# Performance work log

Hardware: AMD Instinct MI355X
Metric: run time of the kernel (lower is better)

Reference implementation:

```python
import jax, jax.numpy as jnp
from jax import lax
import numpy as np

EPS_BN = 1e-5


def _bn(x, g, b, axis):
    # eval-mode BatchNorm with running_mean=0, running_var=1
    shape = [1] * x.ndim
    shape[axis] = -1
    scale = (g / jnp.sqrt(1.0 + EPS_BN)).reshape(shape)
    return x * scale + b.reshape(shape)


def farthest_point_sample(xyz, npoint):
    B, N, _ = xyz.shape
    bidx = jnp.arange(B)

    def body(carry, _):
        dist, far = carry                      # [B,N], [B]
        centroid = xyz[bidx, far]              # [B,3]
        d = jnp.sum((xyz - centroid[:, None, :]) ** 2, axis=-1)
        dist = jnp.minimum(dist, d)
        return (dist, jnp.argmax(dist, axis=-1)), far

    init = (jnp.full((B, N), 1e10, xyz.dtype), jnp.zeros((B,), jnp.int32))
    _, idxs = lax.scan(body, init, None, length=npoint)
    return idxs.T                              # [B,npoint]


def square_distance(src, dst):
    # [B,S,3] x [B,N,3] -> [B,S,N]
    d = -2.0 * jnp.einsum('bsc,bnc->bsn', src, dst)
    d = d + jnp.sum(src ** 2, -1)[:, :, None] + jnp.sum(dst ** 2, -1)[:, None, :]
    return d


def sample_and_group(npoint, nsample, xyz, points):
    B = xyz.shape[0]
    bidx = jnp.arange(B)
    fps_idx = farthest_point_sample(xyz, npoint)          # [B,S]
    new_xyz = xyz[bidx[:, None], fps_idx]                 # [B,S,3]
    new_points = points[bidx[:, None], fps_idx]           # [B,S,C]
    dists = square_distance(new_xyz, xyz)                 # [B,S,N]
    _, idx = lax.top_k(-dists, nsample)                   # nearest nsample
    grouped = points[bidx[:, None, None], idx]            # [B,S,K,C]
    grouped_norm = grouped - new_points[:, :, None, :]
    rep = jnp.broadcast_to(new_points[:, :, None, :], grouped.shape)
    return new_xyz, jnp.concatenate([grouped_norm, rep], axis=-1)  # [B,S,K,2C]


def local_op(x, w, g, b):
    # x [B,S,K,D]; conv1d k=1 over channels D, BN, ReLU, max over K -> [B,out,S]
    y = jnp.einsum('bskd,od->bsko', x, w)
    y = jax.nn.relu(_bn(y, g, b, axis=3))
    y = jnp.max(y, axis=2)                                # [B,S,out]
    return jnp.transpose(y, (0, 2, 1))                    # [B,out,S]


def sa_layer(x, qk_w, v_w, v_b, t_w, t_b, g, b):
    # x [B,C,N]; q and k share weights (offset attention)
    xq = jnp.einsum('bcn,oc->bno', x, qk_w)               # [B,N,C/4]
    xk = jnp.einsum('bcn,oc->bon', x, qk_w)               # [B,C/4,N]
    xv = jnp.einsum('bcn,oc->bon', x, v_w) + v_b[:, None]
    energy = jnp.einsum('bnd,bdm->bnm', xq, xk)           # [B,N,N]
    attn = jax.nn.softmax(energy, axis=-1)
    attn = attn / (1e-9 + attn.sum(axis=1, keepdims=True))
    x_r = jnp.einsum('bcn,bnm->bcm', xv, attn)
    x_r = jnp.einsum('bcn,oc->bon', x - x_r, t_w) + t_b[:, None]
    x_r = jax.nn.relu(_bn(x_r, g, b, axis=1))
    return x + x_r


def setup_inputs() -> dict:
    key = jax.random.key(0)
    ks = iter(jax.random.split(key, 48))
    rn = lambda shape, s=0.05: jax.random.normal(next(ks), shape, jnp.float32) * s
    inp = {
        'xyz': jax.random.normal(next(ks), (32, 16384, 3), jnp.float32),
        'f': jax.random.normal(next(ks), (32, 16384, 3), jnp.float32),
        'conv1_w': rn((64, 6)), 'bn1_g': jnp.ones(64), 'bn1_b': jnp.zeros(64),
        'l0_w': rn((64, 128)), 'l0_g': jnp.ones(64), 'l0_b': jnp.zeros(64),
        'l1_w': rn((64, 128)), 'l1_g': jnp.ones(64), 'l1_b': jnp.zeros(64),
        'st_c1_w': rn((64, 64)), 'st_bn1_g': jnp.ones(64), 'st_bn1_b': jnp.zeros(64),
        'st_c2_w': rn((64, 64)), 'st_bn2_g': jnp.ones(64), 'st_bn2_b': jnp.zeros(64),
        'sa1_qk_w': rn((16, 64)), 'sa1_v_w': rn((64, 64)), 'sa1_v_b': jnp.zeros(64),
        'sa1_t_w': rn((64, 64)), 'sa1_t_b': jnp.zeros(64), 'sa1_g': jnp.ones(64), 'sa1_b': jnp.zeros(64),
        'sa2_qk_w': rn((16, 64)), 'sa2_v_w': rn((64, 64)), 'sa2_v_b': jnp.zeros(64),
        'sa2_t_w': rn((64, 64)), 'sa2_t_b': jnp.zeros(64), 'sa2_g': jnp.ones(64), 'sa2_b': jnp.zeros(64),
        'fuse_w': rn((256, 192)), 'fuse_g': jnp.ones(256), 'fuse_b': jnp.zeros(256),
        'lin1_w': rn((256, 256)), 'bn6_g': jnp.ones(256), 'bn6_b': jnp.zeros(256),
        'lin2_w': rn((256, 256)), 'lin2_b': jnp.zeros(256),
    }
    return inp


def _forward(xyz, f, conv1_w, bn1_g, bn1_b, l0_w, l0_g, l0_b, l1_w, l1_g, l1_b,
             st_c1_w, st_bn1_g, st_bn1_b, st_c2_w, st_bn2_g, st_bn2_b,
             sa1_qk_w, sa1_v_w, sa1_v_b, sa1_t_w, sa1_t_b, sa1_g, sa1_b,
             sa2_qk_w, sa2_v_w, sa2_v_b, sa2_t_w, sa2_t_b, sa2_g, sa2_b,
             fuse_w, fuse_g, fuse_b, lin1_w, bn6_g, bn6_b, lin2_w, lin2_b):
    center = jnp.mean(xyz, axis=1)                        # [B,3]
    xyz_c = xyz - center[:, None, :]
    pts = jnp.concatenate([xyz_c, f], axis=2)             # [B,N,6]
    geo = pts[..., :3]
    xin = jnp.transpose(pts, (0, 2, 1))                   # [B,6,N]
    x = jax.nn.relu(_bn(jnp.einsum('bcn,oc->bon', xin, conv1_w), bn1_g, bn1_b, 1))
    x = jnp.transpose(x, (0, 2, 1))                       # [B,N,64]
    new_xyz, nf = sample_and_group(128, 32, geo, x)
    feature_0 = local_op(nf, l0_w, l0_g, l0_b)            # [B,64,128]
    feature = jnp.transpose(feature_0, (0, 2, 1))
    _, nf2 = sample_and_group(32, 16, new_xyz, feature)
    feature_1 = local_op(nf2, l1_w, l1_g, l1_b)           # [B,64,32]
    # StackedAttention
    x = jax.nn.relu(_bn(jnp.einsum('bcn,oc->bon', feature_1, st_c1_w), st_bn1_g, st_bn1_b, 1))
    x = jax.nn.relu(_bn(jnp.einsum('bcn,oc->bon', x, st_c2_w), st_bn2_g, st_bn2_b, 1))
    x1 = sa_layer(x, sa1_qk_w, sa1_v_w, sa1_v_b, sa1_t_w, sa1_t_b, sa1_g, sa1_b)
    x2 = sa_layer(x1, sa2_qk_w, sa2_v_w, sa2_v_b, sa2_t_w, sa2_t_b, sa2_g, sa2_b)
    x = jnp.concatenate([x1, x2], axis=1)                 # [B,128,32]
    x = jnp.concatenate([x, feature_1], axis=1)           # [B,192,32]
    x = jax.nn.leaky_relu(_bn(jnp.einsum('bcn,oc->bon', x, fuse_w), fuse_g, fuse_b, 1), 0.2)
    x = jnp.max(x, axis=2)                                # [B,256]
    x = jax.nn.relu(_bn(x @ lin1_w.T, bn6_g, bn6_b, 1))   # dropout = identity (eval)
    x = x @ lin2_w.T + lin2_b
    return center, x


def reference(xyz, f, conv1_w, bn1_g, bn1_b, l0_w, l0_g, l0_b, l1_w, l1_g, l1_b,
              st_c1_w, st_bn1_g, st_bn1_b, st_c2_w, st_bn2_g, st_bn2_b,
              sa1_qk_w, sa1_v_w, sa1_v_b, sa1_t_w, sa1_t_b, sa1_g, sa1_b,
              sa2_qk_w, sa2_v_w, sa2_v_b, sa2_t_w, sa2_t_b, sa2_g, sa2_b,
              fuse_w, fuse_g, fuse_b, lin1_w, bn6_g, bn6_b, lin2_w, lin2_b):
    return _forward(xyz, f, conv1_w, bn1_g, bn1_b, l0_w, l0_g, l0_b, l1_w, l1_g, l1_b,
                    st_c1_w, st_bn1_g, st_bn1_b, st_c2_w, st_bn2_g, st_bn2_b,
                    sa1_qk_w, sa1_v_w, sa1_v_b, sa1_t_w, sa1_t_b, sa1_g, sa1_b,
                    sa2_qk_w, sa2_v_w, sa2_v_b, sa2_t_w, sa2_t_b, sa2_g, sa2_b,
                    fuse_w, fuse_g, fuse_b, lin1_w, bn6_g, bn6_b, lin2_w, lin2_b)
```

## Files before the change

kernel.cpp:

```cpp
#include <hip/hip_runtime.h>


__device__ __forceinline__ float bnscale(float g){ return g / sqrtf(1.0f + 1e-5f); }

__device__ __forceinline__ float conv_feat6(float p0,float p1,float p2,float p3,float p4,float p5,
                                            float w0,float w1,float w2,float w3,float w4,float w5,
                                            float sc,float bs){
    float y = p0*w0;
    y = fmaf(p1,w1,y); y = fmaf(p2,w2,y); y = fmaf(p3,w3,y);
    y = fmaf(p4,w4,y); y = fmaf(p5,w5,y);
    return fmaxf(fmaf(y,sc,bs), 0.0f);
}

__device__ __forceinline__ float fpsdist(float dx,float dy,float dz){
    #pragma clang fp contract(off)
    return (dx*dx + dy*dy) + dz*dz;
}

__device__ __forceinline__ float sumsq3(float x,float y,float z){
    #pragma clang fp contract(off)
    return (x*x + y*y) + z*z;
}
__device__ __forceinline__ float sqdist3(float qx,float qy,float qz,float qs,
                                         float px,float py,float pz){
    #pragma clang fp contract(off)
    {
        float dot = (qx*px + qy*py) + qz*pz;
        float pn  = (px*px + py*py) + pz*pz;
        return (-2.0f*dot + qs) + pn;
    }
}

__device__ __forceinline__ unsigned long long packdi(float d, unsigned int idx){
    unsigned int u = __float_as_uint(d);
    unsigned int msk = (unsigned int)((int)u >> 31);
    u ^= (msk | 0x80000000u);
    return ((unsigned long long)u << 32) | (unsigned long long)idx;
}

__device__ __forceinline__ unsigned long long u64min(unsigned long long a, unsigned long long b){
    return a < b ? a : b;
}

__device__ __forceinline__ unsigned long long u64_shfl_down(unsigned long long v, int off){
    unsigned int lo = (unsigned int)v, hi = (unsigned int)(v >> 32);
    lo = __shfl_down(lo, off, 64);
    hi = __shfl_down(hi, off, 64);
    return ((unsigned long long)hi << 32) | (unsigned long long)lo;
}

__device__ __forceinline__ unsigned long long u64_bcast0(unsigned long long v){
    unsigned int lo = (unsigned int)v, hi = (unsigned int)(v >> 32);
    lo = __shfl(lo, 0, 64);
    hi = __shfl(hi, 0, 64);
    return ((unsigned long long)hi << 32) | (unsigned long long)lo;
}

__global__ __launch_bounds__(256) void k_center(const float* __restrict__ xyz,
                                                float* __restrict__ center,
                                                float* __restrict__ out){
    int b = blockIdx.x, t = threadIdx.x;
    __shared__ float sb[256][3];
    float sx=0.f, sy=0.f, sz=0.f;
    for (int n = t; n < 16384; n += 256){
        const float* p = xyz + ((size_t)b*16384 + n)*3;
        sx += p[0]; sy += p[1]; sz += p[2];
    }
    sb[t][0]=sx; sb[t][1]=sy; sb[t][2]=sz;
    __syncthreads();
    for (int off=128; off; off>>=1){
        if (t < off){ sb[t][0]+=sb[t+off][0]; sb[t][1]+=sb[t+off][1]; sb[t][2]+=sb[t+off][2]; }
        __syncthreads();
    }
    if (t < 3){
        float c = sb[0][t] / 16384.0f;
        center[b*3+t] = c;
        out[b*3+t] = c;
    }
}

template<int N, int NPOINT, int NTH, int PPT, bool SUB>
__global__ __launch_bounds__(NTH) void k_fps(const float* __restrict__ src,
                                             const float* __restrict__ center,
                                             int* __restrict__ idx_out){
    static_assert(N == NTH*PPT, "bad fps cfg");
    constexpr int NW = NTH/64;
    int b = blockIdx.x, t = threadIdx.x;
    int wid = t>>6, lane = t&63;

    __shared__ unsigned int s_khi[2][NW], s_klo[2][NW];
    __shared__ float s_wx[2][NW], s_wy[2][NW], s_wz[2][NW];
    __shared__ float s_c0[3];

    float cx0=0.f, cy0=0.f, cz0=0.f;
    if constexpr (SUB){
        cx0 = center[b*3+0]; cy0 = center[b*3+1]; cz0 = center[b*3+2];
    }
    float px[PPT], py[PPT], pz[PPT], dist[PPT];
    #pragma unroll
    for (int i=0;i<PPT;i++){
        int p = t + i*NTH;
        const float* sp = src + ((size_t)b*N + p)*3;
        px[i]=sp[0]-cx0; py[i]=sp[1]-cy0; pz[i]=sp[2]-cz0;
        dist[i]=1e10f;
    }
    if (t==0){
        idx_out[b*NPOINT] = 0;
        s_c0[0]=px[0]; s_c0[1]=py[0]; s_c0[2]=pz[0];
    }
    __syncthreads();
    float cx=s_c0[0], cy=s_c0[1], cz=s_c0[2];

    for (int it=1; it<NPOINT; ++it){
        int par = it & 1;
        float bv = -1.0f; int bi = 0;
        float bx = 0.f, by = 0.f, bz = 0.f;
        #pragma unroll
        for (int i=0;i<PPT;i++){
            float d = fpsdist(px[i]-cx, py[i]-cy, pz[i]-cz);
            float nd = fminf(dist[i], d);
            dist[i] = nd;
            bool better = nd > bv;
            bv = better ? nd : bv;
            bi = better ? (t + i*NTH) : bi;
            bx = better ? px[i] : bx;
            by = better ? py[i] : by;
            bz = better ? pz[i] : bz;
        }
        unsigned long long key = ((unsigned long long)__float_as_uint(bv) << 32)
                               | (unsigned long long)(unsigned)(~(unsigned)bi);
        #pragma unroll
        for (int off=32; off>=1; off>>=1){
            unsigned long long ok = u64_shfl_down(key, off);
            float ox = __shfl_down(bx, off, 64);
            float oy = __shfl_down(by, off, 64);
            float oz = __shfl_down(bz, off, 64);
            bool better = ok > key;
            key = better ? ok : key;
            bx  = better ? ox : bx;
            by  = better ? oy : by;
            bz  = better ? oz : bz;
        }
        if (lane==0){
            s_khi[par][wid] = (unsigned)(key >> 32);
            s_klo[par][wid] = (unsigned)key;
            s_wx[par][wid]  = bx;
            s_wy[par][wid]  = by;
            s_wz[par][wid]  = bz;
        }
        __syncthreads();
        unsigned long long gk = ((unsigned long long)s_khi[par][0] << 32) | s_klo[par][0];
        int gw = 0;
        #pragma unroll
        for (int w2=1; w2<NW; ++w2){
            unsigned long long k2 = ((unsigned long long)s_khi[par][w2] << 32) | s_klo[par][w2];
            if (k2 > gk){ gk = k2; gw = w2; }
        }
        cx = s_wx[par][gw]; cy = s_wy[par][gw]; cz = s_wz[par][gw];
        if (t==0) idx_out[b*NPOINT + it] = (int)(~(unsigned)(gk & 0xFFFFFFFFull));
    }
}

__global__ __launch_bounds__(64) void k_gather1(const float* __restrict__ xyz,
                                                const float* __restrict__ f,
                                                const float* __restrict__ center,
                                                const float* __restrict__ conv1_w,
                                                const float* __restrict__ bn1_g,
                                                const float* __restrict__ bn1_b,
                                                const int* __restrict__ fps_idx,
                                                float* __restrict__ new_xyz,
                                                float* __restrict__ np_feat){
    int q = blockIdx.x; int b = q>>7, s = q&127;
    int o = threadIdx.x;
    int idx = fps_idx[b*128+s];
    const float* xp = xyz + ((size_t)b*16384 + idx)*3;
    const float* fp = f   + ((size_t)b*16384 + idx)*3;
    float p0 = xp[0]-center[b*3+0], p1 = xp[1]-center[b*3+1], p2 = xp[2]-center[b*3+2];
    float p3 = fp[0], p4 = fp[1], p5 = fp[2];
    const float* w = conv1_w + o*6;
    float v = conv_feat6(p0,p1,p2,p3,p4,p5, w[0],w[1],w[2],w[3],w[4],w[5],
                         bnscale(bn1_g[o]), bn1_b[o]);
    np_feat[((size_t)b*128 + s)*64 + o] = v;
    if (o < 3){
        float pc = (o==0)?p0:((o==1)?p1:p2);
        new_xyz[((size_t)b*128 + s)*3 + o] = pc;
    }
}

__global__ __launch_bounds__(256) void k_knn1(const float* __restrict__ xyz,
                                              const float* __restrict__ center,
                                              const float* __restrict__ new_xyz,
                                              int* __restrict__ knn_idx){
    int q = blockIdx.x; int b = q>>7;
    int t = threadIdx.x;
    __shared__ unsigned long long scmin[256];

    float cx = center[b*3+0], cy = center[b*3+1], cz = center[b*3+2];
    float qx = new_xyz[(size_t)q*3+0], qy = new_xyz[(size_t)q*3+1], qz = new_xyz[(size_t)q*3+2];
    float qs = sumsq3(qx,qy,qz);
    const float* xb = xyz + (size_t)b*16384*3;

    unsigned long long m = 0xFFFFFFFFFFFFFFFFull;
    for (int i=0;i<64;i++){
        int n = t + (i<<8);
        const float* p = xb + (size_t)n*3;
        float px = p[0]-cx, py = p[1]-cy, pz = p[2]-cz;
        float d = sqdist3(qx,qy,qz,qs,px,py,pz);
        m = u64min(m, packdi(d, (unsigned)n));
    }
    scmin[t] = m;
    __syncthreads();
    if (t >= 64) return;

    for (int r=0; r<32; ++r){
        unsigned long long mm = u64min(u64min(scmin[t], scmin[t+64]),
                                       u64min(scmin[t+128], scmin[t+192]));
        #pragma unroll
        for (int off=32; off>=1; off>>=1) mm = u64min(mm, u64_shfl_down(mm, off));
        unsigned long long win = u64_bcast0(mm);
        unsigned int widx = (unsigned int)(win & 0xFFFFFFFFull);
        if (t==0) knn_idx[(size_t)q*32 + r] = (int)widx;
        int c = (int)(widx & 255u);
        int n = c + (t<<8);
        const float* p = xb + (size_t)n*3;
        float px = p[0]-cx, py = p[1]-cy, pz = p[2]-cz;
        float d = sqdist3(qx,qy,qz,qs,px,py,pz);
        unsigned long long pk = packdi(d, (unsigned)n);
        if (pk <= win) pk = 0xFFFFFFFFFFFFFFFFull;
        #pragma unroll
        for (int off=32; off>=1; off>>=1) pk = u64min(pk, u64_shfl_down(pk, off));
        if (t==0) scmin[c] = pk;
    }
}

__global__ __launch_bounds__(64) void k_gather2(const float* __restrict__ new_xyz1,
                                                const float* __restrict__ feat,
                                                const int* __restrict__ fps2,
                                                float* __restrict__ new_xyz2,
                                                float* __restrict__ np2){
    int q = blockIdx.x; int b = q>>5, s = q&31;
    int o = threadIdx.x;
    int idx = fps2[b*32+s];
    np2[((size_t)b*32 + s)*64 + o] = feat[((size_t)b*128 + idx)*64 + o];
    if (o < 3) new_xyz2[((size_t)b*32 + s)*3 + o] = new_xyz1[((size_t)b*128 + idx)*3 + o];
}

__global__ __launch_bounds__(256) void k_knn2(const float* __restrict__ pts,
                                              const float* __restrict__ qpts,
                                              int* __restrict__ knn_idx){
    int t = threadIdx.x;
    int wid = t>>6, lane = t&63;
    int q = blockIdx.x*4 + wid;
    int b = q>>5;
    float qx = qpts[(size_t)q*3+0], qy = qpts[(size_t)q*3+1], qz = qpts[(size_t)q*3+2];
    float qs = sumsq3(qx,qy,qz);
    const float* pb = pts + (size_t)b*128*3;

    unsigned long long p0, p1;
    {
        int n = lane;
        float px=pb[n*3+0], py=pb[n*3+1], pz=pb[n*3+2];
        p0 = packdi(sqdist3(qx,qy,qz,qs,px,py,pz), (unsigned)n);
        n = lane + 64;
        px=pb[n*3+0]; py=pb[n*3+1]; pz=pb[n*3+2];
        p1 = packdi(sqdist3(qx,qy,qz,qs,px,py,pz), (unsigned)n);
    }
    for (int r=0; r<16; ++r){
        unsigned long long mm = u64min(p0, p1);
        #pragma unroll
        for (int off=32; off>=1; off>>=1) mm = u64min(mm, u64_shfl_down(mm, off));
        unsigned long long win = u64_bcast0(mm);
        if (lane==0) knn_idx[(size_t)q*16 + r] = (int)(win & 0xFFFFFFFFull);
        if (p0 == win) p0 = 0xFFFFFFFFFFFFFFFFull;
        if (p1 == win) p1 = 0xFFFFFFFFFFFFFFFFull;
    }
}

template<int K, int NQ, int NSRC, bool RECOMP>
__global__ __launch_bounds__(256) void k_group_local(
    const float* __restrict__ xyz, const float* __restrict__ f, const float* __restrict__ center,
    const float* __restrict__ conv1_w, const float* __restrict__ bn1_g, const float* __restrict__ bn1_b,
    const float* __restrict__ src_feat,
    const int* __restrict__ knn_idx, const float* __restrict__ np_feat,
    const float* __restrict__ w, const float* __restrict__ g, const float* __restrict__ bb,
    float* __restrict__ out)
{
    __shared__ float wt[128*65];
    __shared__ float s_sc[64], s_bs[64];
    __shared__ float cwT[6*64];
    __shared__ float s_csc[64], s_cbs[64];
    __shared__ float np_l[4][64];
    __shared__ float gd[4][64];
    __shared__ float s_pts[4][K > 1 ? K : 1][6];
    __shared__ float gdall[RECOMP ? 1 : 4][RECOMP ? 1 : K][64];

    int t = threadIdx.x;
    for (int e=t; e<8192; e+=256){ int o = e>>7, d = e&127; wt[d*65 + o] = w[e]; }
    if (t < 64){ s_sc[t] = bnscale(g[t]); s_bs[t] = bb[t]; }
    if constexpr (RECOMP){
        for (int e=t; e<384; e+=256){ int o = e/6, j = e%6; cwT[j*64 + o] = conv1_w[e]; }
        if (t < 64){ s_csc[t] = bnscale(bn1_g[t]); s_cbs[t] = bn1_b[t]; }
    }
    __syncthreads();

    int wid = t>>6, lane = t&63;
    int q = blockIdx.x*4 + wid;
    int b = q / NQ, s = q % NQ;

    float np_o = np_feat[((size_t)b*NQ + s)*64 + lane];
    np_l[wid][lane] = np_o;

    float C = 0.f;
    #pragma unroll
    for (int d=0; d<64; d++) C = fmaf(np_l[wid][d], wt[(64+d)*65 + lane], C);

    const int* kix = knn_idx + ((size_t)b*NQ + s)*K;
    int myi = kix[lane < K ? lane : 0];

    if constexpr (RECOMP){
        float cx = center[b*3+0], cy = center[b*3+1], cz = center[b*3+2];
        if (lane < K){
            const float* xp = xyz + ((size_t)b*16384 + myi)*3;
            s_pts[wid][lane][0] = xp[0]-cx;
            s_pts[wid][lane][1] = xp[1]-cy;
            s_pts[wid][lane][2] = xp[2]-cz;
            const float* fp = f + ((size_t)b*16384 + myi)*3;
            s_pts[wid][lane][3] = fp[0];
            s_pts[wid][lane][4] = fp[1];
            s_pts[wid][lane][5] = fp[2];
        }
    } else {
        #pragma unroll
        for (int k=0; k<K; ++k){
            int ik = __shfl(myi, k, 64);
            gdall[wid][k][lane] = src_feat[((size_t)b*NSRC + ik)*64 + lane] - np_o;
        }
    }

    float acc = -1e30f;
    #pragma unroll 4
    for (int k=0; k<K; ++k){
        float y = C;
        if constexpr (RECOMP){
            float gv = conv_feat6(s_pts[wid][k][0], s_pts[wid][k][1], s_pts[wid][k][2],
                                  s_pts[wid][k][3], s_pts[wid][k][4], s_pts[wid][k][5],
                                  cwT[0*64+lane], cwT[1*64+lane], cwT[2*64+lane],
                                  cwT[3*64+lane], cwT[4*64+lane], cwT[5*64+lane],
                                  s_csc[lane], s_cbs[lane]);
            gd[wid][lane] = gv - np_o;
            #pragma unroll
            for (int d=0; d<64; d++) y = fmaf(gd[wid][d], wt[d*65 + lane], y);
        } else {
            #pragma unroll
            for (int d=0; d<64; d++) y = fmaf(gdall[wid][k][d], wt[d*65 + lane], y);
        }
        float v = fmaxf(fmaf(y, s_sc[lane], s_bs[lane]), 0.0f);
        acc = fmaxf(acc, v);
    }
    out[((size_t)b*NQ + s)*64 + lane] = acc;
}

__device__ void sa_block(const float* X, float* Xout,
                         float* Q, float* E, float* XV, float* XR, float* CS,
                         const float* qk_w, const float* v_w, const float* v_b,
                         const float* t_w, const float* t_b,
                         const float* g, const float* bb, int t)
{
    for (int e=t; e<512; e+=256){
        int n = e>>4, o = e&15;
        float y = 0.f;
        for (int c=0;c<64;c++) y = fmaf(qk_w[o*64+c], X[c*32+n], y);
        Q[n*16+o] = y;
    }
    for (int e=t; e<2048; e+=256){
        int o = e>>5, n = e&31;
        float y = v_b[o];
        for (int c=0;c<64;c++) y = fmaf(v_w[o*64+c], X[c*32+n], y);
        XV[o*32+n] = y;
    }
    __syncthreads();
    for (int e=t; e<1024; e+=256){
        int n = e>>5, m = e&31;
        float y = 0.f;
        for (int d=0;d<16;d++) y = fmaf(Q[n*16+d], Q[m*16+d], y);
        E[e] = y;
    }
    __syncthreads();
    if (t < 32){
        float mx = -1e30f;
        for (int m=0;m<32;m++) mx = fmaxf(mx, E[t*32+m]);
        float sum = 0.f;
        for (int m=0;m<32;m++){ float v = expf(E[t*32+m]-mx); E[t*32+m]=v; sum += v; }
        for (int m=0;m<32;m++) E[t*32+m] = E[t*32+m] / sum;
    }
    __syncthreads();
    if (t < 32){
        float cs = 0.f;
        for (int n=0;n<32;n++) cs += E[n*32+t];
        CS[t] = 1e-9f + cs;
    }
    __syncthreads();
    for (int e=t; e<1024; e+=256) E[e] = E[e] / CS[e&31];
    __syncthreads();
    for (int e=t; e<2048; e+=256){
        int c = e>>5, m = e&31;
        float y = 0.f;
        for (int n=0;n<32;n++) y = fmaf(XV[c*32+n], E[n*32+m], y);
        XR[c*32+m] = y;
    }
    __syncthreads();
    for (int e=t; e<2048; e+=256){
        int o = e>>5, n = e&31;
        float y = 0.f;
        for (int c=0;c<64;c++) y = fmaf(t_w[o*64+c], X[c*32+n]-XR[c*32+n], y);
        y += t_b[o];
        y = fmaxf(fmaf(y, bnscale(g[o]), bb[o]), 0.0f);
        Xout[e] = X[e] + y;
    }
    __syncthreads();
}

__global__ __launch_bounds__(256) void k_tail(
    const float* __restrict__ f1buf,
    const float* st_c1_w, const float* st_bn1_g, const float* st_bn1_b,
    const float* st_c2_w, const float* st_bn2_g, const float* st_bn2_b,
    const float* sa1_qk, const float* sa1_v, const float* sa1_vb,
    const float* sa1_t, const float* sa1_tb, const float* sa1_g, const float* sa1_b,
    const float* sa2_qk, const float* sa2_v, const float* sa2_vb,
    const float* sa2_t, const float* sa2_tb, const float* sa2_g, const float* sa2_b,
    const float* fuse_w, const float* fuse_g, const float* fuse_b,
    const float* lin1_w, const float* bn6_g, const float* bn6_b,
    const float* lin2_w, const float* lin2_b,
    float* __restrict__ out)
{
    __shared__ float sm[14848];
    float* F1 = sm;
    float* XA = sm + 2048;
    float* XB = sm + 4096;
    float* Q  = sm + 6144;
    float* E  = sm + 6656;
    float* XV = sm + 7680;
    float* XR = sm + 9728;
    float* CS = sm + 11776;
    float* FO = sm + 6144;
    float* PO = sm + 14336;
    float* P2 = sm + 14592;

    int b = blockIdx.x, t = threadIdx.x;

    for (int e=t; e<2048; e+=256){ int n = e>>6, c = e&63; F1[c*32+n] = f1buf[((size_t)b*32+n)*64 + c]; }
    __syncthreads();
    for (int e=t; e<2048; e+=256){
        int o = e>>5, n = e&31;
        float y = 0.f;
        for (int c=0;c<64;c++) y = fmaf(st_c1_w[o*64+c], F1[c*32+n], y);
        XA[e] = fmaxf(fmaf(y, bnscale(st_bn1_g[o]), st_bn1_b[o]), 0.0f);
    }
    __syncthreads();
    for (int e=t; e<2048; e+=256){
        int o = e>>5, n = e&31;
        float y = 0.f;
        for (int c=0;c<64;c++) y = fmaf(st_c2_w[o*64+c], XA[c*32+n], y);
        XB[e] = fmaxf(fmaf(y, bnscale(st_bn2_g[o]), st_bn2_b[o]), 0.0f);
    }
    __syncthreads();
    sa_block(XB, XA, Q,E,XV,XR,CS, sa1_qk, sa1_v, sa1_vb, sa1_t, sa1_tb, sa1_g, sa1_b, t);
    sa_block(XA, XB, Q,E,XV,XR,CS, sa2_qk, sa2_v, sa2_vb, sa2_t, sa2_tb, sa2_g, sa2_b, t);
    for (int e=t; e<8192; e+=256){
        int o = e>>5, n = e&31;
        const float* wr = fuse_w + o*192;
        float y = 0.f;
        for (int c=0;c<64;c++) y = fmaf(wr[c],      XA[c*32+n], y);
        for (int c=0;c<64;c++) y = fmaf(wr[64+c],   XB[c*32+n], y);
        for (int c=0;c<64;c++) y = fmaf(wr[128+c],  F1[c*32+n], y);
        float v = fmaf(y, bnscale(fuse_g[o]), fuse_b[o]);
        FO[e] = (v > 0.0f) ? v : 0.2f*v;
    }
    __syncthreads();
    {
        float mx = -1e30f;
        for (int n=0;n<32;n++) mx = fmaxf(mx, FO[t*32+n]);
        PO[t] = mx;
    }
    __syncthreads();
    {
        const float* wr = lin1_w + t*256;
        float y = 0.f;
        for (int c=0;c<256;c++) y = fmaf(wr[c], PO[c], y);
        P2[t] = fmaxf(fmaf(y, bnscale(bn6_g[t]), bn6_b[t]), 0.0f);
    }
    __syncthreads();
    {
        const float* wr = lin2_w + t*256;
        float y = 0.f;
        for (int c=0;c<256;c++) y = fmaf(wr[c], P2[c], y);
        out[96 + b*256 + t] = y + lin2_b[t];
    }
}

extern "C" void kernel_launch(void* const* d_in, const int* in_sizes, int n_in,
                              void* d_out, int out_size, void* d_ws, size_t ws_size,
                              hipStream_t stream)
{
    const float* xyz      = (const float*)d_in[0];
    const float* f        = (const float*)d_in[1];
    const float* conv1_w  = (const float*)d_in[2];
    const float* bn1_g    = (const float*)d_in[3];
    const float* bn1_b    = (const float*)d_in[4];
    const float* l0_w     = (const float*)d_in[5];
    const float* l0_g     = (const float*)d_in[6];
    const float* l0_b     = (const float*)d_in[7];
    const float* l1_w     = (const float*)d_in[8];
    const float* l1_g     = (const float*)d_in[9];
    const float* l1_b     = (const float*)d_in[10];
    const float* st_c1_w  = (const float*)d_in[11];
    const float* st_bn1_g = (const float*)d_in[12];
    const float* st_bn1_b = (const float*)d_in[13];
    const float* st_c2_w  = (const float*)d_in[14];
    const float* st_bn2_g = (const float*)d_in[15];
    const float* st_bn2_b = (const float*)d_in[16];
    const float* sa1_qk   = (const float*)d_in[17];
    const float* sa1_v    = (const float*)d_in[18];
    const float* sa1_vb   = (const float*)d_in[19];
    const float* sa1_t    = (const float*)d_in[20];
    const float* sa1_tb   = (const float*)d_in[21];
    const float* sa1_g    = (const float*)d_in[22];
    const float* sa1_b    = (const float*)d_in[23];
    const float* sa2_qk   = (const float*)d_in[24];
    const float* sa2_v    = (const float*)d_in[25];
    const float* sa2_vb   = (const float*)d_in[26];
    const float* sa2_t    = (const float*)d_in[27];
    const float* sa2_tb   = (const float*)d_in[28];
    const float* sa2_g    = (const float*)d_in[29];
    const float* sa2_b    = (const float*)d_in[30];
    const float* fuse_w   = (const float*)d_in[31];
    const float* fuse_g   = (const float*)d_in[32];
    const float* fuse_b   = (const float*)d_in[33];
    const float* lin1_w   = (const float*)d_in[34];
    const float* bn6_g    = (const float*)d_in[35];
    const float* bn6_b    = (const float*)d_in[36];
    const float* lin2_w   = (const float*)d_in[37];
    const float* lin2_b   = (const float*)d_in[38];
    float* out = (float*)d_out;

    float* ws = (float*)d_ws;
    float* center   = ws + 0;
    float* new_xyz1 = ws + 96;
    float* np1      = ws + 12384;
    float* feat     = ws + 274528;
    float* new_xyz2 = ws + 536672;
    float* np2      = ws + 539744;
    float* f1       = ws + 605280;
    int*   fps1     = (int*)(ws + 670816);
    int*   knn1     = (int*)(ws + 674912);
    int*   fps2     = (int*)(ws + 805984);
    int*   knn2     = (int*)(ws + 807008);

    k_center<<<32, 256, 0, stream>>>(xyz, center, out);
    k_fps<16384,128,512,32,true><<<32, 512, 0, stream>>>(xyz, center, fps1);
    k_gather1<<<4096, 64, 0, stream>>>(xyz, f, center, conv1_w, bn1_g, bn1_b, fps1, new_xyz1, np1);
    k_knn1<<<4096, 256, 0, stream>>>(xyz, center, new_xyz1, knn1);
    k_group_local<32,128,1,true><<<1024, 256, 0, stream>>>(
        xyz, f, center, conv1_w, bn1_g, bn1_b, nullptr, knn1, np1, l0_w, l0_g, l0_b, feat);
    k_fps<128,32,128,1,false><<<32, 128, 0, stream>>>(new_xyz1, nullptr, fps2);
    k_gather2<<<1024, 64, 0, stream>>>(new_xyz1, feat, fps2, new_xyz2, np2);
    k_knn2<<<256, 256, 0, stream>>>(new_xyz1, new_xyz2, knn2);
    k_group_local<16,32,128,false><<<256, 256, 0, stream>>>(
        nullptr, nullptr, nullptr, nullptr, nullptr, nullptr, feat, knn2, np2, l1_w, l1_g, l1_b, f1);
    k_tail<<<32, 256, 0, stream>>>(f1,
        st_c1_w, st_bn1_g, st_bn1_b, st_c2_w, st_bn2_g, st_bn2_b,
        sa1_qk, sa1_v, sa1_vb, sa1_t, sa1_tb, sa1_g, sa1_b,
        sa2_qk, sa2_v, sa2_vb, sa2_t, sa2_tb, sa2_g, sa2_b,
        fuse_w, fuse_g, fuse_b, lin1_w, bn6_g, bn6_b, lin2_w, lin2_b, out);
}
```

Measured before the change: 763.9 us.

## Fuse centroid into FPS, slim FPS reductions, register-block group_local matmul

```diff
diff --git a/kernel.cpp b/kernel.cpp
--- a/kernel.cpp
+++ b/kernel.cpp
@@ -56,65 +56,54 @@
     return ((unsigned long long)hi << 32) | (unsigned long long)lo;
 }
 
-__global__ __launch_bounds__(256) void k_center(const float* __restrict__ xyz,
-                                                float* __restrict__ center,
-                                                float* __restrict__ out){
+__global__ __launch_bounds__(512, 2) void k_fps1(const float* __restrict__ xyz,
+                                                 float* __restrict__ center,
+                                                 float* __restrict__ out,
+                                                 int* __restrict__ idx_out){
+    constexpr int NTH = 512, PPT = 32, N = 16384, NPOINT = 128, NW = 8;
     int b = blockIdx.x, t = threadIdx.x;
-    __shared__ float sb[256][3];
+    int wid = t>>6, lane = t&63;
+
+    __shared__ float s_red[NW][3];
+    __shared__ unsigned int s_khi[2][NW], s_klo[2][NW];
+
+    const float* xb = xyz + (size_t)b*N*3;
+    float px[PPT], py[PPT], pz[PPT], dist[PPT];
+    #pragma unroll
+    for (int i=0;i<PPT;i++){
+        const float* sp = xb + (size_t)(t + i*NTH)*3;
+        px[i]=sp[0]; py[i]=sp[1]; pz[i]=sp[2];
+        dist[i]=1e10f;
+    }
     float sx=0.f, sy=0.f, sz=0.f;
-    for (int n = t; n < 16384; n += 256){
-        const float* p = xyz + ((size_t)b*16384 + n)*3;
-        sx += p[0]; sy += p[1]; sz += p[2];
-    }
-    sb[t][0]=sx; sb[t][1]=sy; sb[t][2]=sz;
-    __syncthreads();
-    for (int off=128; off; off>>=1){
-        if (t < off){ sb[t][0]+=sb[t+off][0]; sb[t][1]+=sb[t+off][1]; sb[t][2]+=sb[t+off][2]; }
-        __syncthreads();
-    }
+    #pragma unroll
+    for (int i=0;i<PPT;i++){ sx+=px[i]; sy+=py[i]; sz+=pz[i]; }
+    #pragma unroll
+    for (int off=32; off>=1; off>>=1){
+        sx += __shfl_down(sx, off, 64);
+        sy += __shfl_down(sy, off, 64);
+        sz += __shfl_down(sz, off, 64);
+    }
+    if (lane==0){ s_red[wid][0]=sx; s_red[wid][1]=sy; s_red[wid][2]=sz; }
+    __syncthreads();
+    float cx0=0.f, cy0=0.f, cz0=0.f;
+    #pragma unroll
+    for (int w2=0; w2<NW; ++w2){ cx0+=s_red[w2][0]; cy0+=s_red[w2][1]; cz0+=s_red[w2][2]; }
+    cx0 *= (1.0f/16384.0f); cy0 *= (1.0f/16384.0f); cz0 *= (1.0f/16384.0f);
     if (t < 3){
-        float c = sb[0][t] / 16384.0f;
+        float c = (t==0)?cx0:((t==1)?cy0:cz0);
         center[b*3+t] = c;
         out[b*3+t] = c;
     }
-}
-
-template<int N, int NPOINT, int NTH, int PPT, bool SUB>
-__global__ __launch_bounds__(NTH) void k_fps(const float* __restrict__ src,
-                                             const float* __restrict__ center,
-                                             int* __restrict__ idx_out){
-    static_assert(N == NTH*PPT, "bad fps cfg");
-    constexpr int NW = NTH/64;
-    int b = blockIdx.x, t = threadIdx.x;
-    int wid = t>>6, lane = t&63;
-
-    __shared__ unsigned int s_khi[2][NW], s_klo[2][NW];
-    __shared__ float s_wx[2][NW], s_wy[2][NW], s_wz[2][NW];
-    __shared__ float s_c0[3];
-
-    float cx0=0.f, cy0=0.f, cz0=0.f;
-    if constexpr (SUB){
-        cx0 = center[b*3+0]; cy0 = center[b*3+1]; cz0 = center[b*3+2];
-    }
-    float px[PPT], py[PPT], pz[PPT], dist[PPT];
-    #pragma unroll
-    for (int i=0;i<PPT;i++){
-        int p = t + i*NTH;
-        const float* sp = src + ((size_t)b*N + p)*3;
-        px[i]=sp[0]-cx0; py[i]=sp[1]-cy0; pz[i]=sp[2]-cz0;
-        dist[i]=1e10f;
-    }
-    if (t==0){
-        idx_out[b*NPOINT] = 0;
-        s_c0[0]=px[0]; s_c0[1]=py[0]; s_c0[2]=pz[0];
-    }
-    __syncthreads();
-    float cx=s_c0[0], cy=s_c0[1], cz=s_c0[2];
+    #pragma unroll
+    for (int i=0;i<PPT;i++){ px[i]-=cx0; py[i]-=cy0; pz[i]-=cz0; }
+    if (t==0) idx_out[b*NPOINT] = 0;
+
+    float cx = xb[0]-cx0, cy = xb[1]-cy0, cz = xb[2]-cz0;
 
     for (int it=1; it<NPOINT; ++it){
         int par = it & 1;
         float bv = -1.0f; int bi = 0;
-        float bx = 0.f, by = 0.f, bz = 0.f;
         #pragma unroll
         for (int i=0;i<PPT;i++){
             float d = fpsdist(px[i]-cx, py[i]-cy, pz[i]-cz);
@@ -123,6 +112,55 @@
             bool better = nd > bv;
             bv = better ? nd : bv;
             bi = better ? (t + i*NTH) : bi;
+        }
+        unsigned long long key = ((unsigned long long)__float_as_uint(bv) << 32)
+                               | (unsigned long long)(unsigned)(~(unsigned)bi);
+        #pragma unroll
+        for (int off=32; off>=1; off>>=1){
+            unsigned long long ok = u64_shfl_down(key, off);
+            key = ok > key ? ok : key;
+        }
+        if (lane==0){ s_khi[par][wid]=(unsigned)(key>>32); s_klo[par][wid]=(unsigned)key; }
+        __syncthreads();
+        unsigned long long gk = ((unsigned long long)s_khi[par][0] << 32) | s_klo[par][0];
+        #pragma unroll
+        for (int w2=1; w2<NW; ++w2){
+            unsigned long long k2 = ((unsigned long long)s_khi[par][w2] << 32) | s_klo[par][w2];
+            if (k2 > gk) gk = k2;
+        }
+        int gi = (int)(~(unsigned)(gk & 0xFFFFFFFFull));
+        gi = __builtin_amdgcn_readfirstlane(gi);
+        if (t==0) idx_out[b*NPOINT + it] = gi;
+        const float* wp = xb + (size_t)gi*3;
+        cx = wp[0]-cx0; cy = wp[1]-cy0; cz = wp[2]-cz0;
+    }
+}
+
+__global__ __launch_bounds__(64) void k_fps2(const float* __restrict__ pts,
+                                             int* __restrict__ idx_out){
+    int b = blockIdx.x, lane = threadIdx.x;
+    const float* pb = pts + (size_t)b*128*3;
+    float px[2],py[2],pz[2],dist[2];
+    #pragma unroll
+    for (int i=0;i<2;i++){
+        const float* sp = pb + (size_t)(lane + i*64)*3;
+        px[i]=sp[0]; py[i]=sp[1]; pz[i]=sp[2];
+        dist[i]=1e10f;
+    }
+    if (lane==0) idx_out[b*32] = 0;
+    float cx=pb[0], cy=pb[1], cz=pb[2];
+
+    for (int it=1; it<32; ++it){
+        float bv=-1.0f; int bi=0;
+        float bx=0.f, by=0.f, bz=0.f;
+        #pragma unroll
+        for (int i=0;i<2;i++){
+            float d = fpsdist(px[i]-cx, py[i]-cy, pz[i]-cz);
+            float nd = fminf(dist[i], d);
+            dist[i]=nd;
+            bool better = nd > bv;
+            bv = better ? nd : bv;
+            bi = better ? (lane + i*64) : bi;
             bx = better ? px[i] : bx;
             by = better ? py[i] : by;
             bz = better ? pz[i] : bz;
@@ -137,27 +175,13 @@
             float oz = __shfl_down(bz, off, 64);
             bool better = ok > key;
             key = better ? ok : key;
-            bx  = better ? ox : bx;
-            by  = better ? oy : by;
-            bz  = better ? oz : bz;
-        }
-        if (lane==0){
-            s_khi[par][wid] = (unsigned)(key >> 32);
-            s_klo[par][wid] = (unsigned)key;
-            s_wx[par][wid]  = bx;
-            s_wy[par][wid]  = by;
-            s_wz[par][wid]  = bz;
-        }
-        __syncthreads();
-        unsigned long long gk = ((unsigned long long)s_khi[par][0] << 32) | s_klo[par][0];
-        int gw = 0;
-        #pragma unroll
-        for (int w2=1; w2<NW; ++w2){
-            unsigned long long k2 = ((unsigned long long)s_khi[par][w2] << 32) | s_klo[par][w2];
-            if (k2 > gk){ gk = k2; gw = w2; }
-        }
-        cx = s_wx[par][gw]; cy = s_wy[par][gw]; cz = s_wz[par][gw];
-        if (t==0) idx_out[b*NPOINT + it] = (int)(~(unsigned)(gk & 0xFFFFFFFFull));
+            bx = better ? ox : bx;
+            by = better ? oy : by;
+            bz = better ? oz : bz;
+        }
+        key = u64_bcast0(key);
+        cx = __shfl(bx, 0, 64); cy = __shfl(by, 0, 64); cz = __shfl(bz, 0, 64);
+        if (lane==0) idx_out[b*32 + it] = (int)(~(unsigned)(key & 0xFFFFFFFFull));
     }
 }
 
@@ -277,7 +301,7 @@
 }
 
 template<int K, int NQ, int NSRC, bool RECOMP>
-__global__ __launch_bounds__(256) void k_group_local(
+__global__ __launch_bounds__(256, 2) void k_group_local(
     const float* __restrict__ xyz, const float* __restrict__ f, const float* __restrict__ center,
     const float* __restrict__ conv1_w, const float* __restrict__ bn1_g, const float* __restrict__ bn1_b,
     const float* __restrict__ src_feat,
@@ -290,9 +314,8 @@
     __shared__ float cwT[6*64];
     __shared__ float s_csc[64], s_cbs[64];
     __shared__ float np_l[4][64];
-    __shared__ float gd[4][64];
-    __shared__ float s_pts[4][K > 1 ? K : 1][6];
-    __shared__ float gdall[RECOMP ? 1 : 4][RECOMP ? 1 : K][64];
+    __shared__ float gda[4][K][64];
+    __shared__ float s_pts[4][K][6];
 
     int t = threadIdx.x;
     for (int e=t; e<8192; e+=256){ int o = e>>7, d = e&127; wt[d*65 + o] = w[e]; }
@@ -310,16 +333,12 @@
     float np_o = np_feat[((size_t)b*NQ + s)*64 + lane];
     np_l[wid][lane] = np_o;
 
-    float C = 0.f;
-    #pragma unroll
-    for (int d=0; d<64; d++) C = fmaf(np_l[wid][d], wt[(64+d)*65 + lane], C);
-
     const int* kix = knn_idx + ((size_t)b*NQ + s)*K;
-    int myi = kix[lane < K ? lane : 0];
 
     if constexpr (RECOMP){
         float cx = center[b*3+0], cy = center[b*3+1], cz = center[b*3+2];
         if (lane < K){
+            int myi = kix[lane];
             const float* xp = xyz + ((size_t)b*16384 + myi)*3;
             s_pts[wid][lane][0] = xp[0]-cx;
             s_pts[wid][lane][1] = xp[1]-cy;
@@ -329,32 +348,57 @@
             s_pts[wid][lane][4] = fp[1];
             s_pts[wid][lane][5] = fp[2];
         }
-    } else {
         #pragma unroll
         for (int k=0; k<K; ++k){
-            int ik = __shfl(myi, k, 64);
-            gdall[wid][k][lane] = src_feat[((size_t)b*NSRC + ik)*64 + lane] - np_o;
-        }
-    }
-
-    float acc = -1e30f;
-    #pragma unroll 4
-    for (int k=0; k<K; ++k){
-        float y = C;
-        if constexpr (RECOMP){
             float gv = conv_feat6(s_pts[wid][k][0], s_pts[wid][k][1], s_pts[wid][k][2],
                                   s_pts[wid][k][3], s_pts[wid][k][4], s_pts[wid][k][5],
                                   cwT[0*64+lane], cwT[1*64+lane], cwT[2*64+lane],
                                   cwT[3*64+lane], cwT[4*64+lane], cwT[5*64+lane],
                                   s_csc[lane], s_cbs[lane]);
-            gd[wid][lane] = gv - np_o;
+            gda[wid][k][lane] = gv - np_o;
+        }
+    } else {
+        int myi = kix[lane < K ? lane : 0];
+        #pragma unroll
+        for (int k=0; k<K; ++k){
+            int ik = __shfl(myi, k, 64);
+            gda[wid][k][lane] = src_feat[((size_t)b*NSRC + ik)*64 + lane] - np_o;
+        }
+    }
+
+    float C = 0.f;
+    #pragma unroll
+    for (int d=0; d<64; d++) C = fmaf(np_l[wid][d], wt[(64+d)*65 + lane], C);
+
+    float acc_y[K];
+    #pragma unroll
+    for (int k=0;k<K;k++) acc_y[k] = C;
+
+    #pragma unroll
+    for (int c=0; c<2; ++c){
+        float wr[32];
+        #pragma unroll
+        for (int j=0;j<32;j++) wr[j] = wt[(c*32+j)*65 + lane];
+        #pragma unroll
+        for (int k=0;k<K;k++){
+            const float4* g4 = (const float4*)&gda[wid][k][c*32];
+            float yk = 0.f;
             #pragma unroll
-            for (int d=0; d<64; d++) y = fmaf(gd[wid][d], wt[d*65 + lane], y);
-        } else {
-            #pragma unroll
-            for (int d=0; d<64; d++) y = fmaf(gdall[wid][k][d], wt[d*65 + lane], y);
-        }
-        float v = fmaxf(fmaf(y, s_sc[lane], s_bs[lane]), 0.0f);
+            for (int j4=0;j4<8;j4++){
+                float4 gg = g4[j4];
+                yk = fmaf(gg.x, wr[j4*4+0], yk);
+                yk = fmaf(gg.y, wr[j4*4+1], yk);
+                yk = fmaf(gg.z, wr[j4*4+2], yk);
+                yk = fmaf(gg.w, wr[j4*4+3], yk);
+            }
+            acc_y[k] = acc_y[k] + yk;
+        }
+    }
+
+    float acc = -1e30f;
+    #pragma unroll
+    for (int k=0;k<K;k++){
+        float v = fmaxf(fmaf(acc_y[k], s_sc[lane], s_bs[lane]), 0.0f);
         acc = fmaxf(acc, v);
     }
     out[((size_t)b*NQ + s)*64 + lane] = acc;
@@ -556,13 +600,12 @@
     int*   fps2     = (int*)(ws + 805984);
     int*   knn2     = (int*)(ws + 807008);
 
-    k_center<<<32, 256, 0, stream>>>(xyz, center, out);
-    k_fps<16384,128,512,32,true><<<32, 512, 0, stream>>>(xyz, center, fps1);
+    k_fps1<<<32, 512, 0, stream>>>(xyz, center, out, fps1);
     k_gather1<<<4096, 64, 0, stream>>>(xyz, f, center, conv1_w, bn1_g, bn1_b, fps1, new_xyz1, np1);
     k_knn1<<<4096, 256, 0, stream>>>(xyz, center, new_xyz1, knn1);
     k_group_local<32,128,1,true><<<1024, 256, 0, stream>>>(
         xyz, f, center, conv1_w, bn1_g, bn1_b, nullptr, knn1, np1, l0_w, l0_g, l0_b, feat);
-    k_fps<128,32,128,1,false><<<32, 128, 0, stream>>>(new_xyz1, nullptr, fps2);
+    k_fps2<<<32, 64, 0, stream>>>(new_xyz1, fps2);
     k_gather2<<<1024, 64, 0, stream>>>(new_xyz1, feat, fps2, new_xyz2, np2);
     k_knn2<<<256, 256, 0, stream>>>(new_xyz1, new_xyz2, knn2);
     k_group_local<16,32,128,false><<<256, 256, 0, stream>>>(
```

Result: faster. 651.9 us (-14.7%).
